# Kernel optimization log

Measured on AMD Instinct MI355X. Metric: run time of the kernel, lower is better.

The kernel has to match this reference:

```python
import jax, jax.numpy as jnp
import numpy as np

T = 2048      # number of utterances in the dialogue (sequential loop dim)
L = 50        # tokens per utterance
V = 30000     # vocab size
D = 300       # word embedding dim
NF = 64       # CNN filters per width
H = 100       # hidden size (hard-coded in CMN)
NC = 7        # emotion classes
WIND = 40     # args.wind1 sliding memory window
HOPS = 3      # args.hops
NEG = -1e10   # masked_fill value in dotprod_attention


def setup_inputs() -> dict:
    key = jax.random.key(0)
    ks = jax.random.split(key, 24)
    s = 0.05

    def n(k, shape):
        return jax.random.normal(k, shape, jnp.float32) * s

    return {
        "sents": jax.random.randint(ks[0], (T, L), 0, V, dtype=jnp.int32),
        "lengths": jax.random.randint(ks[1], (T,), 1, L, dtype=jnp.int32),
        "emb": n(ks[2], (V, D)),
        "Wc3": n(ks[3], (NF, 1, 3, D)), "bc3": n(ks[4], (NF,)),
        "Wc4": n(ks[5], (NF, 1, 4, D)), "bc4": n(ks[6], (NF,)),
        "Wc5": n(ks[7], (NF, 1, 5, D)), "bc5": n(ks[8], (NF,)),
        "Wt": n(ks[9], (3 * NF, H)), "bt": n(ks[10], (H,)),
        "Wih_c": n(ks[11], (3 * H, H)), "Whh_c": n(ks[12], (3 * H, H)),
        "bih_c": n(ks[13], (3 * H,)), "bhh_c": n(ks[14], (3 * H,)),
        "Wih_m": n(ks[15], (3 * H, H)), "Whh_m": n(ks[16], (3 * H, H)),
        "bih_m": n(ks[17], (3 * H,)), "bhh_m": n(ks[18], (3 * H,)),
        "Wcls": n(ks[19], (H, NC)), "bcls": n(ks[20], (NC,)),
    }


def _gru_cell(x, h, Wih, Whh, bih, bhh):
    # torch GRU cell, gate order (r, z, n)
    gi = x @ Wih.T + bih
    gh = h @ Whh.T + bhh
    ir, iz, inn = jnp.split(gi, 3, axis=-1)
    hr, hz, hn = jnp.split(gh, 3, axis=-1)
    r = jax.nn.sigmoid(ir + hr)
    z = jax.nn.sigmoid(iz + hz)
    nw = jnp.tanh(inn + r * hn)
    return (1.0 - z) * nw + z * h


def reference(sents, lengths, emb, Wc3, bc3, Wc4, bc4, Wc5, bc5, Wt, bt,
              Wih_c, Whh_c, bih_c, bhh_c, Wih_m, Whh_m, bih_m, bhh_m,
              Wcls, bcls):
    # ---- CNN utterance encoder (dropout layers are identity in eval) ----
    w = emb[sents]                       # (T, L, D)
    x = w[:, None]                       # (T, 1, L, D)  NCHW
    feats = []
    for Wc, bc in ((Wc3, bc3), (Wc4, bc4), (Wc5, bc5)):
        y = jax.lax.conv_general_dilated(
            x, Wc, window_strides=(1, 1), padding='VALID',
            dimension_numbers=('NCHW', 'OIHW', 'NCHW'))  # (T, NF, L-fs+1, 1)
        feats.append(jnp.max(jax.nn.relu(y + bc[None, :, None, None]), axis=(2, 3)))
    s_utt = jnp.tanh(jnp.concatenate(feats, axis=1) @ Wt + bt)  # (T, H)

    # ---- context GRU over utterances 0..T-2 (hidden after torch step i is hiddens[i-1]) ----
    def cont_step(h, u):
        h2 = _gru_cell(u, h, Wih_c, Whh_c, bih_c, bhh_c)
        return h2, h2
    _, hiddens = jax.lax.scan(cont_step, jnp.zeros((H,), jnp.float32), s_utt[:-1])  # (T-1, H)

    # ---- sliding memory windows: step i (1..T-1) sees hiddens[i-WIND .. i-1], newest last ----
    idx = jnp.arange(1, T)[:, None] - WIND + jnp.arange(WIND)[None, :]  # (T-1, WIND)
    valid = idx >= 0
    mem_all = jnp.where(valid[..., None], hiddens[jnp.clip(idx, 0)], 0.0)  # (T-1, WIND, H)

    def attend(query, mem, v):
        # query: (H,), mem: (WIND, H), v: (WIND,) bool
        for _ in range(HOPS):
            scores = jnp.where(v, mem @ query, NEG)
            a = jax.nn.softmax(scores)
            query = jnp.tanh(query + a @ mem)
            if HOPS > 1:
                # mem_gru over the valid suffix of the window (zero init hidden,
                # padded slots skipped so recurrence starts at first valid slot)
                def mstep(hm, xv):
                    xx, vv = xv
                    hn = _gru_cell(xx, hm, Wih_m, Whh_m, bih_m, bhh_m)
                    hm = jnp.where(vv, hn, hm)
                    return hm, hm
                _, mem = jax.lax.scan(mstep, jnp.zeros((H,), jnp.float32), (mem, v))
        return query

    queries = jax.vmap(attend)(s_utt[1:], mem_all, valid)       # (T-1, H)
    s_cont = jnp.concatenate([s_utt[:1], queries], axis=0)      # (T, H)
    logits = s_cont @ Wcls + bcls                                # (T, NC)
    return jax.nn.log_softmax(logits, axis=1)
```

## Files before the change

kernel.cpp:

```cpp
#include <hip/hip_runtime.h>

#define TT 2048
#define LL 50
#define DD 300
#define HH 100
#define NCC 7

typedef unsigned short u16;
typedef unsigned int u32;
typedef _Float16 f16x2 __attribute__((ext_vector_type(2)));
typedef _Float16 f16x8 __attribute__((ext_vector_type(8)));
typedef float f32x4 __attribute__((ext_vector_type(4)));

__device__ __forceinline__ float frcp(float x){ return __builtin_amdgcn_rcpf(x); }
__device__ __forceinline__ float sigm(float x){ return frcp(1.f + __expf(-x)); }
__device__ __forceinline__ float ftanh(float x){ return 1.f - 2.f * frcp(1.f + __expf(2.f * x)); }

#if defined(__has_builtin)
#if __has_builtin(__builtin_amdgcn_fdot2)
#define HAS_FDOT2 1
#endif
#endif
__device__ __forceinline__ float fdot2(f16x2 a, f16x2 b, float c){
#ifdef HAS_FDOT2
  return __builtin_amdgcn_fdot2(a, b, c, false);
#else
  return c + (float)a.x * (float)b.x + (float)a.y * (float)b.y;
#endif
}
__device__ __forceinline__ f16x2 pk(float x, float y){ f16x2 r; r.x = (_Float16)x; r.y = (_Float16)y; return r; }

__global__ __launch_bounds__(256) void k_prep(const float* __restrict__ Wc3,
    const float* __restrict__ Wc4, const float* __restrict__ Wc5, _Float16* __restrict__ wtp)
{
  const int t = blockIdx.x;
  int kki, ntile, kt;
  if (t < 120){ kki = 0; ntile = t / 30;        kt = t % 30; }
  else if (t < 280){ kki = 1; int r = t - 120; ntile = r / 40; kt = r % 40; }
  else { kki = 2; int r = t - 280;             ntile = r / 50; kt = r % 50; }
  const float* W = (kki == 0) ? Wc3 : ((kki == 1) ? Wc4 : Wc5);
  const int kk = 3 + kki;
  #pragma unroll
  for (int u = 0; u < 2; ++u){
    int e = threadIdx.x * 2 + u;
    int lane = e >> 3, i = e & 7;
    int k = kt * 32 + (lane >> 4) * 8 + i;
    int f = ntile * 16 + (lane & 15);
    int j = k / 320, d = k - j * 320;
    float v = (d < DD) ? W[((size_t)f * kk + j) * DD + d] : 0.f;
    wtp[(size_t)t * 512 + e] = (_Float16)v;
  }
}

#define WST 328
__global__ __launch_bounds__(256) void k_cnn(const int* __restrict__ sents,
    const float* __restrict__ emb, const _Float16* __restrict__ wtp,
    const float* __restrict__ bc3, const float* __restrict__ bc4, const float* __restrict__ bc5,
    const float* __restrict__ Wt,  const float* __restrict__ bt,
    float* __restrict__ su)
{
  __shared__ __attribute__((aligned(16))) _Float16 w16[52 * WST];
  __shared__ float feats[192];
  __shared__ int ids[LL];
  const int tid = threadIdx.x;
  const int s = blockIdx.x;

  if (tid < LL) ids[tid] = sents[s * LL + tid];
  for (int e = tid; e < 52 * WST / 2; e += 256) ((u32*)w16)[e] = 0u;
  __syncthreads();
  for (int e = tid; e < LL * 75; e += 256){
    int l = e / 75, d4 = (e - l * 75) * 4;
    float4 v = *(const float4*)&emb[(size_t)ids[l] * DD + d4];
    _Float16* p = &w16[l * WST + d4];
    p[0] = (_Float16)v.x; p[1] = (_Float16)v.y; p[2] = (_Float16)v.z; p[3] = (_Float16)v.w;
  }
  __syncthreads();

  const int lane = tid & 63, wid = tid >> 6;
  const int rl = lane & 15, gp = lane >> 4;
  const int kkstart[3] = {0, 120, 280};
  float fmaxv[3];
  #pragma unroll
  for (int kki = 0; kki < 3; ++kki){
    const int kk = 3 + kki, nkt = kk * 10, Pk = LL - kk + 1;
    f32x4 acc0 = {0.f,0.f,0.f,0.f}, acc1 = acc0, acc2 = acc0;
    const f16x8* bp = (const f16x8*)(wtp + (size_t)(kkstart[kki] + wid * nkt) * 512) + lane;
    int j = 0, d = gp * 8;
    for (int kt = 0; kt < nkt; ++kt){
      f16x8 b  = bp[(size_t)kt * 64];
      f16x8 a0 = *(const f16x8*)&w16[(rl      + j) * WST + d];
      f16x8 a1 = *(const f16x8*)&w16[(16 + rl + j) * WST + d];
      f16x8 a2 = *(const f16x8*)&w16[(32 + rl + j) * WST + d];
      acc0 = __builtin_amdgcn_mfma_f32_16x16x32_f16(a0, b, acc0, 0, 0, 0);
      acc1 = __builtin_amdgcn_mfma_f32_16x16x32_f16(a1, b, acc1, 0, 0, 0);
      acc2 = __builtin_amdgcn_mfma_f32_16x16x32_f16(a2, b, acc2, 0, 0, 0);
      d += 32; if (d >= 320){ d -= 320; ++j; }
    }
    float m = -1e30f;
    #pragma unroll
    for (int r = 0; r < 4; ++r){
      int p0 = gp * 4 + r;
      if (p0 < Pk)      m = fmaxf(m, acc0[r]);
      if (16 + p0 < Pk) m = fmaxf(m, acc1[r]);
      if (32 + p0 < Pk) m = fmaxf(m, acc2[r]);
    }
    m = fmaxf(m, __shfl_xor(m, 16));
    m = fmaxf(m, __shfl_xor(m, 32));
    fmaxv[kki] = m;
  }
  if (lane < 16){
    feats[  0 + wid * 16 + lane] = fmaxv[0];
    feats[ 64 + wid * 16 + lane] = fmaxv[1];
    feats[128 + wid * 16 + lane] = fmaxv[2];
  }
  __syncthreads();
  if (tid < 192){
    float bias = (tid < 64) ? bc3[tid] : ((tid < 128) ? bc4[tid - 64] : bc5[tid - 128]);
    feats[tid] = fmaxf(0.f, feats[tid] + bias);
  }
  __syncthreads();
  if (tid < HH){
    float acc = bt[tid];
    for (int c = 0; c < 192; ++c)
      acc += feats[c] * Wt[c * HH + tid];
    su[(size_t)s * HH + tid] = ftanh(acc);
  }
}

__global__ __launch_bounds__(320) void k_gi(const float* __restrict__ src,
    const float* __restrict__ W, const float* __restrict__ b, float* __restrict__ dst)
{
  __shared__ float x[HH];
  const int t = blockIdx.x, tid = threadIdx.x;
  if (tid < HH) x[tid] = src[(size_t)t * HH + tid];
  __syncthreads();
  if (tid < 300){
    float acc = b[tid];
    const float* wr = W + (size_t)tid * HH;
    #pragma unroll
    for (int i = 0; i < 25; ++i){
      float4 wv = *(const float4*)(wr + 4 * i);
      float4 xv = *(const float4*)&x[4 * i];
      acc += xv.x * wv.x + xv.y * wv.y + xv.z * wv.z + xv.w * wv.w;
    }
    dst[(size_t)t * 300 + tid] = acc;
  }
}

#define CH 32
__global__ __launch_bounds__(320, 1) void k_scan(const float* __restrict__ gi,
    const float* __restrict__ Whh, const float* __restrict__ bhh,
    float* __restrict__ hid, int steps)
{
  __shared__ __attribute__((aligned(16))) _Float16 h16[128];
  __shared__ __attribute__((aligned(16))) float gh_l[304];
  __shared__ float gi_buf[CH * 300];
  __shared__ float hid_buf[CH * HH];
  const int tid = threadIdx.x;
  const int lane = tid & 63, wvid = tid >> 6;
  const int rl = lane & 15, gp = lane >> 4;

  f16x8 afrag[4][4];
  #pragma unroll
  for (int m = 0; m < 4; ++m){
    int mt = wvid + 5 * m;
    int row = mt * 16 + rl;
    #pragma unroll
    for (int kt = 0; kt < 4; ++kt){
      f16x8 f;
      #pragma unroll
      for (int i = 0; i < 8; ++i){
        int k = kt * 32 + gp * 8 + i;
        float v = (row < 300 && k < 100) ? Whh[(size_t)row * 100 + k] : 0.f;
        f[i] = (_Float16)v;
      }
      afrag[m][kt] = f;
    }
  }
  float bhr = 0.f, bhz = 0.f, bhn = 0.f, hreg = 0.f;
  if (tid < HH){ bhr = bhh[tid]; bhz = bhh[tid + 100]; bhn = bhh[tid + 200]; }
  if (tid < 128) h16[tid] = (_Float16)0.f;
  {
    int c0 = (steps < CH ? steps : CH) * 75;
    for (int e = tid; e < c0; e += 320)
      ((float4*)gi_buf)[e] = ((const float4*)gi)[e];
  }
  __syncthreads();

  int t0 = 0;
  while (t0 < steps){
    int cnt = steps - t0; if (cnt > CH) cnt = CH;
    for (int s = 0; s < cnt; ++s){
      {
        const f16x8* hp = (const f16x8*)h16;
        f16x8 bf0 = hp[ 0 + gp], bf1 = hp[ 4 + gp], bf2 = hp[ 8 + gp], bf3 = hp[12 + gp];
        #pragma unroll
        for (int m = 0; m < 4; ++m){
          f32x4 acc = {0.f, 0.f, 0.f, 0.f};
          acc = __builtin_amdgcn_mfma_f32_16x16x32_f16(afrag[m][0], bf0, acc, 0, 0, 0);
          acc = __builtin_amdgcn_mfma_f32_16x16x32_f16(afrag[m][1], bf1, acc, 0, 0, 0);
          acc = __builtin_amdgcn_mfma_f32_16x16x32_f16(afrag[m][2], bf2, acc, 0, 0, 0);
          acc = __builtin_amdgcn_mfma_f32_16x16x32_f16(afrag[m][3], bf3, acc, 0, 0, 0);
          int mt = wvid + 5 * m;
          if (rl == 0 && mt < 19)
            *(float4*)&gh_l[mt * 16 + gp * 4] = *(float4*)&acc;
        }
      }
      __syncthreads();
      if (tid < HH){
        const float* gpp = gi_buf + s * 300;
        float r = sigm(gpp[tid]       + gh_l[tid]       + bhr);
        float z = sigm(gpp[tid + 100] + gh_l[tid + 100] + bhz);
        float n = ftanh(gpp[tid + 200] + r * (gh_l[tid + 200] + bhn));
        float o = (1.f - z) * n + z * hreg;
        hreg = o;
        h16[tid] = (_Float16)o;
        hid_buf[s * HH + tid] = o;
      }
      __syncthreads();
    }
    for (int e = tid; e < cnt * 25; e += 320)
      ((float4*)(hid + (size_t)t0 * HH))[e] = ((const float4*)hid_buf)[e];
    int nt0 = t0 + cnt;
    int ncnt = steps - nt0; if (ncnt > CH) ncnt = CH; if (ncnt < 0) ncnt = 0;
    for (int e = tid; e < ncnt * 75; e += 320)
      ((float4*)gi_buf)[e] = ((const float4*)(gi + (size_t)nt0 * 300))[e];
    __syncthreads();
    t0 = nt0;
  }
}

__global__ __launch_bounds__(320) void k_att(
    const float* __restrict__ su, const float* __restrict__ hid, const float* __restrict__ gm,
    const float* __restrict__ Wih, const float* __restrict__ Whh,
    const float* __restrict__ bih, const float* __restrict__ bhh,
    float* __restrict__ scont)
{
  __shared__ float mem_l[40 * 104];
  __shared__ __attribute__((aligned(16))) _Float16 mem16[40 * 104];
  __shared__ float hbuf[HH];
  __shared__ __attribute__((aligned(16))) _Float16 hb16[104];
  __shared__ float gh_l[300];
  __shared__ float q_l[104];
  __shared__ float sc_l[40];
  __shared__ float bi_l[300];
  __shared__ _Float16 g_l[40 * 300];
  const int tid = threadIdx.x;
  const int q = blockIdx.x;
  int wmin = 39 - q; if (wmin < 0) wmin = 0;
  f16x2 wreg[52];
  float bh = 0.f;

  if (tid < 300){ bi_l[tid] = bih[tid]; bh = bhh[tid]; }
  if (tid < 104) q_l[tid] = (tid < 100) ? su[(size_t)(q + 1) * HH + tid] : 0.f;
  for (int e = tid; e < 40 * 104; e += 320){
    int w = e / 104, i = e - w * 104;
    float v = 0.f;
    if (i < 100 && w >= wmin) v = hid[(size_t)(q - 39 + w) * HH + i];
    mem_l[e] = v;
    mem16[e] = (_Float16)v;
  }
  for (int e = tid; e < 40 * 300; e += 320){
    int w = e / 300, j = e - w * 300;
    float v = (w >= wmin) ? gm[(size_t)(q - 39 + w) * 300 + j] : 0.f;
    g_l[e] = (_Float16)v;
  }
  if (tid < 300){
    const float* r0 = Whh + (size_t)tid * 100;
    #pragma unroll
    for (int i = 0; i < 25; ++i){
      float4 a = *(const float4*)(r0 + 4 * i);
      wreg[2*i] = pk(a.x, a.y); wreg[2*i+1] = pk(a.z, a.w);
    }
  }
  wreg[50] = pk(0,0); wreg[51] = pk(0,0);
  __syncthreads();

  for (int hop = 0; hop < 3; ++hop){
    if (tid < 40){
      float a0 = 0, a1 = 0, a2 = 0, a3 = 0;
      const float* mr = &mem_l[tid * 104];
      #pragma unroll
      for (int i = 0; i < 25; ++i){
        float4 m4 = *(const float4*)&mr[4 * i];
        float4 q4 = *(const float4*)&q_l[4 * i];
        a0 += m4.x * q4.x; a1 += m4.y * q4.y; a2 += m4.z * q4.z; a3 += m4.w * q4.w;
      }
      sc_l[tid] = (tid >= wmin) ? ((a0 + a1) + (a2 + a3)) : -1e10f;
    }
    __syncthreads();
    if (tid < 64){
      float v = (tid < 40) ? sc_l[tid] : -3e38f;
      float m = v;
      #pragma unroll
      for (int off = 32; off; off >>= 1) m = fmaxf(m, __shfl_xor(m, off));
      float e = (tid < 40) ? __expf(v - m) : 0.f;
      float ssum = e;
      #pragma unroll
      for (int off = 32; off; off >>= 1) ssum += __shfl_xor(ssum, off);
      if (tid < 40) sc_l[tid] = e * frcp(ssum);
    }
    __syncthreads();
    if (tid < 50){
      float c0 = 0.f, c1 = 0.f;
      for (int w = wmin; w < 40; ++w){
        float a = sc_l[w];
        float2 mv = *(const float2*)&mem_l[w * 104 + 2 * tid];
        c0 += a * mv.x; c1 += a * mv.y;
      }
      float q0 = ftanh(q_l[2 * tid]     + c0);
      float q1 = ftanh(q_l[2 * tid + 1] + c1);
      *(float2*)&q_l[2 * tid] = make_float2(q0, q1);
      if (hop == 2)
        *(float2*)&scont[(size_t)(q + 1) * HH + 2 * tid] = make_float2(q0, q1);
    }
    if (hop == 2) break;

    if (hop == 1){
      if (tid < 300){
        const float* r0 = Wih + (size_t)tid * 100;
        #pragma unroll
        for (int i = 0; i < 25; ++i){
          float4 a = *(const float4*)(r0 + 4 * i);
          wreg[2*i] = pk(a.x, a.y); wreg[2*i+1] = pk(a.z, a.w);
        }
        for (int w = 0; w < 40; ++w){
          float a0 = 0, a1 = 0;
          const float4* mq = (const float4*)&mem16[w * 104];
          #pragma unroll
          for (int g = 0; g < 13; ++g){
            float4 hv = mq[g];
            a0 = fdot2(wreg[4*g  ], __builtin_bit_cast(f16x2, hv.x), a0);
            a1 = fdot2(wreg[4*g+1], __builtin_bit_cast(f16x2, hv.y), a1);
            a0 = fdot2(wreg[4*g+2], __builtin_bit_cast(f16x2, hv.z), a0);
            a1 = fdot2(wreg[4*g+3], __builtin_bit_cast(f16x2, hv.w), a1);
          }
          g_l[w * 300 + tid] = (_Float16)(a0 + a1 + bi_l[tid]);
        }
        const float* rh = Whh + (size_t)tid * 100;
        #pragma unroll
        for (int i = 0; i < 25; ++i){
          float4 a = *(const float4*)(rh + 4 * i);
          wreg[2*i] = pk(a.x, a.y); wreg[2*i+1] = pk(a.z, a.w);
        }
      }
    }

    if (tid < HH) hbuf[tid] = 0.f;
    if (tid < 104) hb16[tid] = (_Float16)0.f;
    __syncthreads();
    for (int w = 0; w < 40; ++w){
      if (tid < 300){
        float a0 = 0, a1 = 0;
        const float4* hq = (const float4*)hb16;
        #pragma unroll
        for (int g = 0; g < 13; ++g){
          float4 hv = hq[g];
          a0 = fdot2(wreg[4*g  ], __builtin_bit_cast(f16x2, hv.x), a0);
          a1 = fdot2(wreg[4*g+1], __builtin_bit_cast(f16x2, hv.y), a1);
          a0 = fdot2(wreg[4*g+2], __builtin_bit_cast(f16x2, hv.z), a0);
          a1 = fdot2(wreg[4*g+3], __builtin_bit_cast(f16x2, hv.w), a1);
        }
        gh_l[tid] = a0 + a1 + bh;
      }
      __syncthreads();
      if (tid < HH){
        float o = hbuf[tid];
        if (w >= wmin){
          const _Float16* gp = &g_l[w * 300];
          float gir = (float)gp[tid], giz = (float)gp[tid + 100], gin = (float)gp[tid + 200];
          float r = sigm(gir + gh_l[tid]);
          float z = sigm(giz + gh_l[tid + 100]);
          float n = ftanh(gin + r * gh_l[tid + 200]);
          o = (1.f - z) * n + z * o;
        }
        hbuf[tid] = o;
        hb16[tid] = (_Float16)o;
        mem_l[w * 104 + tid] = o;
        mem16[w * 104 + tid] = (_Float16)o;
      }
      __syncthreads();
    }
  }
}

__global__ __launch_bounds__(256) void k_cls(const float* __restrict__ su, const float* __restrict__ scont,
    const float* __restrict__ Wcls, const float* __restrict__ bcls, float* __restrict__ out)
{
  __shared__ float wl[HH * NCC];
  __shared__ float bl[NCC];
  const int tid = threadIdx.x;
  for (int e = tid; e < HH * NCC; e += 256) wl[e] = Wcls[e];
  if (tid < NCC) bl[tid] = bcls[tid];
  __syncthreads();
  int r = blockIdx.x * 256 + tid;
  if (r < TT){
    const float* v = (r == 0) ? su : (scont + (size_t)r * HH);
    float l[NCC];
    #pragma unroll
    for (int c = 0; c < NCC; ++c) l[c] = bl[c];
    for (int h = 0; h < HH; ++h){
      float x = v[h];
      #pragma unroll
      for (int c = 0; c < NCC; ++c) l[c] += x * wl[h * NCC + c];
    }
    float m = l[0];
    #pragma unroll
    for (int c = 1; c < NCC; ++c) m = fmaxf(m, l[c]);
    float ssum = 0.f;
    #pragma unroll
    for (int c = 0; c < NCC; ++c) ssum += __expf(l[c] - m);
    float lse = m + __logf(ssum);
    #pragma unroll
    for (int c = 0; c < NCC; ++c) out[(size_t)r * NCC + c] = l[c] - lse;
  }
}

extern "C" void kernel_launch(void* const* d_in, const int* in_sizes, int n_in,
                              void* d_out, int out_size, void* d_ws, size_t ws_size,
                              hipStream_t stream)
{
  const int* sents  = (const int*)d_in[0];
  const float* emb    = (const float*)d_in[2];
  const float* Wc3    = (const float*)d_in[3];  const float* bc3 = (const float*)d_in[4];
  const float* Wc4    = (const float*)d_in[5];  const float* bc4 = (const float*)d_in[6];
  const float* Wc5    = (const float*)d_in[7];  const float* bc5 = (const float*)d_in[8];
  const float* Wt     = (const float*)d_in[9];  const float* bt  = (const float*)d_in[10];
  const float* Wih_c  = (const float*)d_in[11]; const float* Whh_c = (const float*)d_in[12];
  const float* bih_c  = (const float*)d_in[13]; const float* bhh_c = (const float*)d_in[14];
  const float* Wih_m  = (const float*)d_in[15]; const float* Whh_m = (const float*)d_in[16];
  const float* bih_m  = (const float*)d_in[17]; const float* bhh_m = (const float*)d_in[18];
  const float* Wcls   = (const float*)d_in[19]; const float* bcls  = (const float*)d_in[20];

  float* ws    = (float*)d_ws;
  float* su    = ws;
  float* gic   = su  + 204800;
  float* hid   = gic + 614100;
  float* gm    = gic;
  float* scont = hid + 204700;
  _Float16* wtp = (_Float16*)(scont + 204800);

  k_prep<<<480,     256, 0, stream>>>(Wc3, Wc4, Wc5, wtp);
  k_cnn <<<TT,      256, 0, stream>>>(sents, emb, wtp, bc3, bc4, bc5, Wt, bt, su);
  k_gi  <<<TT - 1,  320, 0, stream>>>(su, Wih_c, bih_c, gic);
  k_scan<<<1,       320, 0, stream>>>(gic, Whh_c, bhh_c, hid, TT - 1);
  k_gi  <<<TT - 1,  320, 0, stream>>>(hid, Wih_m, bih_m, gm);
  k_att <<<TT - 1,  320, 0, stream>>>(su, hid, gm, Wih_m, Whh_m, bih_m, bhh_m, scont);
  k_cls <<<(TT + 255) / 256, 256, 0, stream>>>(su, scont, Wcls, bcls, (float*)d_out);
}
```

Before: 2.011 ms.

## Interleave GRU gate rows so each lane computes its hidden unit from MFMA output

Reorders the Whh rows loaded into MFMA A-fragments so each 4-row group holds the r, z and n rows of one hidden unit. Each lane can then finish the GRU gate math straight from its accumulator registers instead of staging gh through shared memory. The hidden state is double-buffered, which drops one __syncthreads per recurrent step. In exchange every wave issues 20 MFMAs per step instead of 16, and the gate math is computed redundantly across lanes.

Result: slower. 2.435 ms (+21.1%).

```diff
diff --git a/kernel.cpp b/kernel.cpp
--- a/kernel.cpp
+++ b/kernel.cpp
@@ -152,34 +152,36 @@
     const float* __restrict__ Whh, const float* __restrict__ bhh,
     float* __restrict__ hid, int steps)
 {
-  __shared__ __attribute__((aligned(16))) _Float16 h16[128];
-  __shared__ __attribute__((aligned(16))) float gh_l[304];
+  __shared__ __attribute__((aligned(16))) _Float16 hA[128];
+  __shared__ __attribute__((aligned(16))) _Float16 hB[128];
   __shared__ float gi_buf[CH * 300];
   __shared__ float hid_buf[CH * HH];
   const int tid = threadIdx.x;
   const int lane = tid & 63, wvid = tid >> 6;
   const int rl = lane & 15, gp = lane >> 4;
 
-  f16x8 afrag[4][4];
+  f16x8 afrag[5][4];
   #pragma unroll
-  for (int m = 0; m < 4; ++m){
-    int mt = wvid + 5 * m;
-    int row = mt * 16 + rl;
+  for (int m = 0; m < 5; ++m){
+    const int mt = wvid * 5 + m;
+    const int uu = mt * 4 + (rl >> 2), g = rl & 3;
     #pragma unroll
     for (int kt = 0; kt < 4; ++kt){
       f16x8 f;
       #pragma unroll
       for (int i = 0; i < 8; ++i){
         int k = kt * 32 + gp * 8 + i;
-        float v = (row < 300 && k < 100) ? Whh[(size_t)row * 100 + k] : 0.f;
+        float v = (g < 3 && k < 100) ? Whh[(size_t)(uu + 100 * g) * 100 + k] : 0.f;
         f[i] = (_Float16)v;
       }
       afrag[m][kt] = f;
     }
   }
-  float bhr = 0.f, bhz = 0.f, bhn = 0.f, hreg = 0.f;
-  if (tid < HH){ bhr = bhh[tid]; bhz = bhh[tid + 100]; bhn = bhh[tid + 200]; }
-  if (tid < 128) h16[tid] = (_Float16)0.f;
+  const int msel = rl % 5;
+  const int u = wvid * 20 + msel * 4 + gp;
+  const float bhr = bhh[u], bhz = bhh[u + 100], bhn = bhh[u + 200];
+  float hreg = 0.f;
+  if (tid < 128){ hA[tid] = (_Float16)0.f; hB[tid] = (_Float16)0.f; }
   {
     int c0 = (steps < CH ? steps : CH) * 75;
     for (int e = tid; e < c0; e += 320)
@@ -191,31 +193,46 @@
   while (t0 < steps){
     int cnt = steps - t0; if (cnt > CH) cnt = CH;
     for (int s = 0; s < cnt; ++s){
-      {
-        const f16x8* hp = (const f16x8*)h16;
-        f16x8 bf0 = hp[ 0 + gp], bf1 = hp[ 4 + gp], bf2 = hp[ 8 + gp], bf3 = hp[12 + gp];
-        #pragma unroll
-        for (int m = 0; m < 4; ++m){
-          f32x4 acc = {0.f, 0.f, 0.f, 0.f};
-          acc = __builtin_amdgcn_mfma_f32_16x16x32_f16(afrag[m][0], bf0, acc, 0, 0, 0);
-          acc = __builtin_amdgcn_mfma_f32_16x16x32_f16(afrag[m][1], bf1, acc, 0, 0, 0);
-          acc = __builtin_amdgcn_mfma_f32_16x16x32_f16(afrag[m][2], bf2, acc, 0, 0, 0);
-          acc = __builtin_amdgcn_mfma_f32_16x16x32_f16(afrag[m][3], bf3, acc, 0, 0, 0);
-          int mt = wvid + 5 * m;
-          if (rl == 0 && mt < 19)
-            *(float4*)&gh_l[mt * 16 + gp * 4] = *(float4*)&acc;
-        }
-      }
-      __syncthreads();
-      if (tid < HH){
-        const float* gpp = gi_buf + s * 300;
-        float r = sigm(gpp[tid]       + gh_l[tid]       + bhr);
-        float z = sigm(gpp[tid + 100] + gh_l[tid + 100] + bhz);
-        float n = ftanh(gpp[tid + 200] + r * (gh_l[tid + 200] + bhn));
-        float o = (1.f - z) * n + z * hreg;
-        hreg = o;
-        h16[tid] = (_Float16)o;
-        hid_buf[s * HH + tid] = o;
+      const int st = t0 + s;
+      const _Float16* hs = (st & 1) ? hB : hA;
+      _Float16*       hd = (st & 1) ? hA : hB;
+      float gir = gi_buf[s * 300 + u];
+      float giz = gi_buf[s * 300 + 100 + u];
+      float gin = gi_buf[s * 300 + 200 + u];
+      const f16x8* hp = (const f16x8*)hs;
+      f16x8 bf0 = hp[0 + gp], bf1 = hp[4 + gp], bf2 = hp[8 + gp], bf3 = hp[12 + gp];
+      f32x4 a0 = {0.f,0.f,0.f,0.f}, a1 = a0, a2 = a0, a3 = a0, a4 = a0;
+      a0 = __builtin_amdgcn_mfma_f32_16x16x32_f16(afrag[0][0], bf0, a0, 0, 0, 0);
+      a1 = __builtin_amdgcn_mfma_f32_16x16x32_f16(afrag[1][0], bf0, a1, 0, 0, 0);
+      a2 = __builtin_amdgcn_mfma_f32_16x16x32_f16(afrag[2][0], bf0, a2, 0, 0, 0);
+      a3 = __builtin_amdgcn_mfma_f32_16x16x32_f16(afrag[3][0], bf0, a3, 0, 0, 0);
+      a4 = __builtin_amdgcn_mfma_f32_16x16x32_f16(afrag[4][0], bf0, a4, 0, 0, 0);
+      a0 = __builtin_amdgcn_mfma_f32_16x16x32_f16(afrag[0][1], bf1, a0, 0, 0, 0);
+      a1 = __builtin_amdgcn_mfma_f32_16x16x32_f16(afrag[1][1], bf1, a1, 0, 0, 0);
+      a2 = __builtin_amdgcn_mfma_f32_16x16x32_f16(afrag[2][1], bf1, a2, 0, 0, 0);
+      a3 = __builtin_amdgcn_mfma_f32_16x16x32_f16(afrag[3][1], bf1, a3, 0, 0, 0);
+      a4 = __builtin_amdgcn_mfma_f32_16x16x32_f16(afrag[4][1], bf1, a4, 0, 0, 0);
+      a0 = __builtin_amdgcn_mfma_f32_16x16x32_f16(afrag[0][2], bf2, a0, 0, 0, 0);
+      a1 = __builtin_amdgcn_mfma_f32_16x16x32_f16(afrag[1][2], bf2, a1, 0, 0, 0);
+      a2 = __builtin_amdgcn_mfma_f32_16x16x32_f16(afrag[2][2], bf2, a2, 0, 0, 0);
+      a3 = __builtin_amdgcn_mfma_f32_16x16x32_f16(afrag[3][2], bf2, a3, 0, 0, 0);
+      a4 = __builtin_amdgcn_mfma_f32_16x16x32_f16(afrag[4][2], bf2, a4, 0, 0, 0);
+      a0 = __builtin_amdgcn_mfma_f32_16x16x32_f16(afrag[0][3], bf3, a0, 0, 0, 0);
+      a1 = __builtin_amdgcn_mfma_f32_16x16x32_f16(afrag[1][3], bf3, a1, 0, 0, 0);
+      a2 = __builtin_amdgcn_mfma_f32_16x16x32_f16(afrag[2][3], bf3, a2, 0, 0, 0);
+      a3 = __builtin_amdgcn_mfma_f32_16x16x32_f16(afrag[3][3], bf3, a3, 0, 0, 0);
+      a4 = __builtin_amdgcn_mfma_f32_16x16x32_f16(afrag[4][3], bf3, a4, 0, 0, 0);
+      float ghr = msel==0 ? a0[0] : msel==1 ? a1[0] : msel==2 ? a2[0] : msel==3 ? a3[0] : a4[0];
+      float ghz = msel==0 ? a0[1] : msel==1 ? a1[1] : msel==2 ? a2[1] : msel==3 ? a3[1] : a4[1];
+      float ghn = msel==0 ? a0[2] : msel==1 ? a1[2] : msel==2 ? a2[2] : msel==3 ? a3[2] : a4[2];
+      float r = sigm(gir + ghr + bhr);
+      float z = sigm(giz + ghz + bhz);
+      float n = ftanh(gin + r * (ghn + bhn));
+      float o = (1.f - z) * n + z * hreg;
+      hreg = o;
+      if (rl < 5){
+        hd[u] = (_Float16)o;
+        hid_buf[s * HH + u] = o;
       }
       __syncthreads();
     }
```

## Batch eight queries per block in attention kernel and run memory GRU on MFMA

Applied to the files above, without the earlier changes.

The per-query attention kernel is replaced by one that handles eight queries per block. Their memory-GRU recurrences are batched into 16x16x32 f16 MFMA matmuls, with Whh held in registers in a pre-packed MFMA layout produced by a new prep kernel. The hop-1 input projection also moves to MFMA, using chunked staging of gate inputs and a double-buffered hidden state in shared memory. This is meant to replace the many tiny per-block fdot2 matvecs and their 40 sequential syncs per hop with fewer, denser matrix ops. In exchange, memory is now stored in f16, which loosens precision, and launching 256 blocks at one block per CU limits parallelism.

After: 1.744 ms. 13.3% less time.

```diff
diff --git a/kernel.cpp b/kernel.cpp
--- a/kernel.cpp
+++ b/kernel.cpp
@@ -9,6 +9,7 @@
 typedef unsigned short u16;
 typedef unsigned int u32;
 typedef _Float16 f16x2 __attribute__((ext_vector_type(2)));
+typedef _Float16 f16x4 __attribute__((ext_vector_type(4)));
 typedef _Float16 f16x8 __attribute__((ext_vector_type(8)));
 typedef float f32x4 __attribute__((ext_vector_type(4)));
 
@@ -49,6 +50,22 @@
     int j = k / 320, d = k - j * 320;
     float v = (d < DD) ? W[((size_t)f * kk + j) * DD + d] : 0.f;
     wtp[(size_t)t * 512 + e] = (_Float16)v;
+  }
+}
+
+__global__ __launch_bounds__(256) void k_prep2(const float* __restrict__ Whh,
+    const float* __restrict__ Wih, _Float16* __restrict__ wpkW, _Float16* __restrict__ wpkI)
+{
+  const float* W = (blockIdx.x == 0) ? Whh : Wih;
+  _Float16* dst  = (blockIdx.x == 0) ? wpkW : wpkI;
+  for (int idx = threadIdx.x; idx < 28 * 4 * 64 * 8; idx += 256){
+    int i = idx & 7, lane = (idx >> 3) & 63, kt = (idx >> 9) & 3, mt = idx >> 11;
+    int rl = lane & 15, gp = lane >> 4;
+    int p = mt * 16 + rl;
+    int k = kt * 32 + gp * 8 + i;
+    int uu = p >> 2, g = p & 3;
+    float v = (mt < 25 && g < 3 && k < 100) ? W[(size_t)(uu + 100 * g) * 100 + k] : 0.f;
+    dst[idx] = (_Float16)v;
   }
 }
 
@@ -230,156 +247,209 @@
   }
 }
 
-__global__ __launch_bounds__(320) void k_att(
+__global__ __launch_bounds__(256, 1) void k_att2(
     const float* __restrict__ su, const float* __restrict__ hid, const float* __restrict__ gm,
-    const float* __restrict__ Wih, const float* __restrict__ Whh,
+    const _Float16* __restrict__ wpkW, const _Float16* __restrict__ wpkI,
     const float* __restrict__ bih, const float* __restrict__ bhh,
     float* __restrict__ scont)
 {
-  __shared__ float mem_l[40 * 104];
-  __shared__ __attribute__((aligned(16))) _Float16 mem16[40 * 104];
-  __shared__ float hbuf[HH];
-  __shared__ __attribute__((aligned(16))) _Float16 hb16[104];
-  __shared__ float gh_l[300];
-  __shared__ float q_l[104];
-  __shared__ float sc_l[40];
-  __shared__ float bi_l[300];
-  __shared__ _Float16 g_l[40 * 300];
+  __shared__ __attribute__((aligned(16))) _Float16 MEM[40][8][136];
+  __shared__ __attribute__((aligned(16))) _Float16 H16[2][8][136];
+  __shared__ __attribute__((aligned(16))) _Float16 GI2[8][8][100][4];
+  __shared__ float QL[8][104];
+  __shared__ float SC[8][40];
+
   const int tid = threadIdx.x;
-  const int q = blockIdx.x;
-  int wmin = 39 - q; if (wmin < 0) wmin = 0;
-  f16x2 wreg[52];
-  float bh = 0.f;
-
-  if (tid < 300){ bi_l[tid] = bih[tid]; bh = bhh[tid]; }
-  if (tid < 104) q_l[tid] = (tid < 100) ? su[(size_t)(q + 1) * HH + tid] : 0.f;
-  for (int e = tid; e < 40 * 104; e += 320){
-    int w = e / 104, i = e - w * 104;
-    float v = 0.f;
-    if (i < 100 && w >= wmin) v = hid[(size_t)(q - 39 + w) * HH + i];
-    mem_l[e] = v;
-    mem16[e] = (_Float16)v;
-  }
-  for (int e = tid; e < 40 * 300; e += 320){
-    int w = e / 300, j = e - w * 300;
-    float v = (w >= wmin) ? gm[(size_t)(q - 39 + w) * 300 + j] : 0.f;
-    g_l[e] = (_Float16)v;
-  }
-  if (tid < 300){
-    const float* r0 = Whh + (size_t)tid * 100;
-    #pragma unroll
-    for (int i = 0; i < 25; ++i){
-      float4 a = *(const float4*)(r0 + 4 * i);
-      wreg[2*i] = pk(a.x, a.y); wreg[2*i+1] = pk(a.z, a.w);
-    }
-  }
-  wreg[50] = pk(0,0); wreg[51] = pk(0,0);
+  const int lane = tid & 63, wvid = tid >> 6;
+  const int rl = lane & 15, gp = lane >> 4;
+  const int qbase = blockIdx.x * 8;
+  const int j = rl & 7;
+  const int qi = qbase + j;
+  int wminj = 39 - qi; if (wminj < 0) wminj = 0;
+  if (qi >= TT - 1) wminj = 40;
+
+  f16x8 aW[7][4];
+  #pragma unroll
+  for (int t = 0; t < 7; ++t){
+    int mt = wvid + 4 * t;
+    #pragma unroll
+    for (int kt = 0; kt < 4; ++kt)
+      aW[t][kt] = *(const f16x8*)(wpkW + (size_t)((mt * 4 + kt) * 64 + lane) * 8);
+  }
+  float bi_[7][3];
+  #pragma unroll
+  for (int t = 0; t < 7; ++t){
+    int mt = wvid + 4 * t;
+    bool v = (mt < 25);
+    int uu = v ? (mt * 4 + gp) : 0;
+    bi_[t][0] = v ? bih[uu]       : 0.f;
+    bi_[t][1] = v ? bih[uu + 100] : 0.f;
+    bi_[t][2] = v ? bih[uu + 200] : 0.f;
+  }
+  const int cbase = (rl < 8) ? 0 : 4;
+  float bh_[4][3]; int cu[4]; bool cv[4];
+  #pragma unroll
+  for (int tt = 0; tt < 4; ++tt){
+    int t = cbase + tt;
+    int mt = wvid + 4 * t;
+    bool v = (t < 7) && (mt < 25);
+    cv[tt] = v;
+    int uu = v ? (mt * 4 + gp) : 0;
+    cu[tt] = uu;
+    bh_[tt][0] = v ? bhh[uu]       : 0.f;
+    bh_[tt][1] = v ? bhh[uu + 100] : 0.f;
+    bh_[tt][2] = v ? bhh[uu + 200] : 0.f;
+  }
+
+  for (int e = tid; e < 40 * 8 * 34; e += 256){
+    int i4 = e % 34, wj = e / 34, w = wj >> 3, jj = wj & 7;
+    int qq = qbase + jj;
+    int row = qq - 39 + w;
+    f16x4 v4 = {0, 0, 0, 0};
+    if (i4 < 25 && qq < TT - 1 && row >= 0){
+      float4 f = *(const float4*)&hid[(size_t)row * HH + i4 * 4];
+      v4[0] = (_Float16)f.x; v4[1] = (_Float16)f.y; v4[2] = (_Float16)f.z; v4[3] = (_Float16)f.w;
+    }
+    *(f16x4*)&MEM[w][jj][i4 * 4] = v4;
+  }
+  for (int e = tid; e < 8 * 104; e += 256){
+    int jj = e / 104, ii = e % 104;
+    int qq = qbase + jj;
+    QL[jj][ii] = (ii < 100 && qq < TT - 1) ? su[(size_t)(qq + 1) * HH + ii] : 0.f;
+  }
+  for (int e = tid; e < 2 * 8 * 136; e += 256) ((_Float16*)H16)[e] = (_Float16)0;
   __syncthreads();
 
   for (int hop = 0; hop < 3; ++hop){
-    if (tid < 40){
-      float a0 = 0, a1 = 0, a2 = 0, a3 = 0;
-      const float* mr = &mem_l[tid * 104];
-      #pragma unroll
-      for (int i = 0; i < 25; ++i){
-        float4 m4 = *(const float4*)&mr[4 * i];
-        float4 q4 = *(const float4*)&q_l[4 * i];
-        a0 += m4.x * q4.x; a1 += m4.y * q4.y; a2 += m4.z * q4.z; a3 += m4.w * q4.w;
-      }
-      sc_l[tid] = (tid >= wmin) ? ((a0 + a1) + (a2 + a3)) : -1e10f;
-    }
-    __syncthreads();
-    if (tid < 64){
-      float v = (tid < 40) ? sc_l[tid] : -3e38f;
-      float m = v;
-      #pragma unroll
-      for (int off = 32; off; off >>= 1) m = fmaxf(m, __shfl_xor(m, off));
-      float e = (tid < 40) ? __expf(v - m) : 0.f;
-      float ssum = e;
-      #pragma unroll
-      for (int off = 32; off; off >>= 1) ssum += __shfl_xor(ssum, off);
-      if (tid < 40) sc_l[tid] = e * frcp(ssum);
-    }
-    __syncthreads();
-    if (tid < 50){
-      float c0 = 0.f, c1 = 0.f;
-      for (int w = wmin; w < 40; ++w){
-        float a = sc_l[w];
-        float2 mv = *(const float2*)&mem_l[w * 104 + 2 * tid];
-        c0 += a * mv.x; c1 += a * mv.y;
-      }
-      float q0 = ftanh(q_l[2 * tid]     + c0);
-      float q1 = ftanh(q_l[2 * tid + 1] + c1);
-      *(float2*)&q_l[2 * tid] = make_float2(q0, q1);
-      if (hop == 2)
-        *(float2*)&scont[(size_t)(q + 1) * HH + 2 * tid] = make_float2(q0, q1);
-    }
-    if (hop == 2) break;
-
-    if (hop == 1){
-      if (tid < 300){
-        const float* r0 = Wih + (size_t)tid * 100;
-        #pragma unroll
-        for (int i = 0; i < 25; ++i){
-          float4 a = *(const float4*)(r0 + 4 * i);
-          wreg[2*i] = pk(a.x, a.y); wreg[2*i+1] = pk(a.z, a.w);
-        }
-        for (int w = 0; w < 40; ++w){
-          float a0 = 0, a1 = 0;
-          const float4* mq = (const float4*)&mem16[w * 104];
-          #pragma unroll
-          for (int g = 0; g < 13; ++g){
-            float4 hv = mq[g];
-            a0 = fdot2(wreg[4*g  ], __builtin_bit_cast(f16x2, hv.x), a0);
-            a1 = fdot2(wreg[4*g+1], __builtin_bit_cast(f16x2, hv.y), a1);
-            a0 = fdot2(wreg[4*g+2], __builtin_bit_cast(f16x2, hv.z), a0);
-            a1 = fdot2(wreg[4*g+3], __builtin_bit_cast(f16x2, hv.w), a1);
-          }
-          g_l[w * 300 + tid] = (_Float16)(a0 + a1 + bi_l[tid]);
-        }
-        const float* rh = Whh + (size_t)tid * 100;
-        #pragma unroll
-        for (int i = 0; i < 25; ++i){
-          float4 a = *(const float4*)(rh + 4 * i);
-          wreg[2*i] = pk(a.x, a.y); wreg[2*i+1] = pk(a.z, a.w);
-        }
-      }
-    }
-
-    if (tid < HH) hbuf[tid] = 0.f;
-    if (tid < 104) hb16[tid] = (_Float16)0.f;
-    __syncthreads();
-    for (int w = 0; w < 40; ++w){
-      if (tid < 300){
-        float a0 = 0, a1 = 0;
-        const float4* hq = (const float4*)hb16;
+    for (int e = tid; e < 320; e += 256){
+      int jj = e / 40, w = e % 40;
+      int qq = qbase + jj;
+      int wm = 39 - qq; if (wm < 0) wm = 0; if (qq >= TT - 1) wm = 40;
+      float acc = 0.f;
+      if (w >= wm){
         #pragma unroll
         for (int g = 0; g < 13; ++g){
-          float4 hv = hq[g];
-          a0 = fdot2(wreg[4*g  ], __builtin_bit_cast(f16x2, hv.x), a0);
-          a1 = fdot2(wreg[4*g+1], __builtin_bit_cast(f16x2, hv.y), a1);
-          a0 = fdot2(wreg[4*g+2], __builtin_bit_cast(f16x2, hv.z), a0);
-          a1 = fdot2(wreg[4*g+3], __builtin_bit_cast(f16x2, hv.w), a1);
+          f16x8 m8 = *(const f16x8*)&MEM[w][jj][g * 8];
+          const float* qp = &QL[jj][g * 8];
+          #pragma unroll
+          for (int i = 0; i < 8; ++i) acc += (float)m8[i] * qp[i];
         }
-        gh_l[tid] = a0 + a1 + bh;
+        SC[jj][w] = acc;
+      } else SC[jj][w] = -1e10f;
+    }
+    __syncthreads();
+    if (tid < 8){
+      float m = -3e38f;
+      for (int w = 0; w < 40; ++w) m = fmaxf(m, SC[tid][w]);
+      float s = 0.f;
+      for (int w = 0; w < 40; ++w){ float e = __expf(SC[tid][w] - m); SC[tid][w] = e; s += e; }
+      float inv = frcp(s);
+      for (int w = 0; w < 40; ++w) SC[tid][w] *= inv;
+    }
+    __syncthreads();
+    for (int e = tid; e < 400; e += 256){
+      int jj = e / 50, i2 = e % 50;
+      float c0 = 0.f, c1 = 0.f;
+      for (int w = 0; w < 40; ++w){
+        float a = SC[jj][w];
+        f16x2 m2 = *(const f16x2*)&MEM[w][jj][i2 * 2];
+        c0 += a * (float)m2.x; c1 += a * (float)m2.y;
+      }
+      float q0 = ftanh(QL[jj][i2 * 2]     + c0);
+      float q1 = ftanh(QL[jj][i2 * 2 + 1] + c1);
+      QL[jj][i2 * 2] = q0; QL[jj][i2 * 2 + 1] = q1;
+      if (hop == 2){
+        int qq = qbase + jj;
+        if (qq < TT - 1)
+          *(float2*)&scont[(size_t)(qq + 1) * HH + i2 * 2] = make_float2(q0, q1);
+      }
+    }
+    if (hop == 2) break;
+    for (int e = tid; e < 800; e += 256) H16[0][e / 100][e % 100] = (_Float16)0;
+    float hrg[4] = {0.f, 0.f, 0.f, 0.f};
+    __syncthreads();
+
+    for (int c = 0; c < 5; ++c){
+      if (hop == 0){
+        for (int e = tid; e < 6400; e += 256){
+          int s8 = e / 800, jj = (e / 100) & 7, uu = e % 100;
+          int qq = qbase + jj;
+          int row = qq - 39 + c * 8 + s8;
+          f16x4 g4 = {0, 0, 0, 0};
+          if (qq < TT - 1 && row >= 0){
+            const float* gr = &gm[(size_t)row * 300];
+            g4[0] = (_Float16)gr[uu]; g4[1] = (_Float16)gr[uu + 100]; g4[2] = (_Float16)gr[uu + 200];
+          }
+          *(f16x4*)&GI2[s8][jj][uu][0] = g4;
+        }
+      } else {
+        #pragma unroll
+        for (int nt = 0; nt < 4; ++nt){
+          f16x8 bf[4];
+          #pragma unroll
+          for (int kt = 0; kt < 4; ++kt)
+            bf[kt] = *(const f16x8*)&MEM[c * 8 + nt * 2 + (rl >> 3)][rl & 7][kt * 32 + gp * 8];
+          #pragma unroll
+          for (int t = 0; t < 7; ++t){
+            int mt = wvid + 4 * t;
+            if (mt < 25){
+              f32x4 ac = {0.f, 0.f, 0.f, 0.f};
+              #pragma unroll
+              for (int kt = 0; kt < 4; ++kt){
+                f16x8 ai = *(const f16x8*)(wpkI + (size_t)((mt * 4 + kt) * 64 + lane) * 8);
+                ac = __builtin_amdgcn_mfma_f32_16x16x32_f16(ai, bf[kt], ac, 0, 0, 0);
+              }
+              int uu = mt * 4 + gp;
+              int s8 = nt * 2 + (rl >> 3), jj = rl & 7;
+              f16x4 g4;
+              g4[0] = (_Float16)(ac[0] + bi_[t][0]);
+              g4[1] = (_Float16)(ac[1] + bi_[t][1]);
+              g4[2] = (_Float16)(ac[2] + bi_[t][2]);
+              g4[3] = (_Float16)0.f;
+              *(f16x4*)&GI2[s8][jj][uu][0] = g4;
+            }
+          }
+        }
       }
       __syncthreads();
-      if (tid < HH){
-        float o = hbuf[tid];
-        if (w >= wmin){
-          const _Float16* gp = &g_l[w * 300];
-          float gir = (float)gp[tid], giz = (float)gp[tid + 100], gin = (float)gp[tid + 200];
-          float r = sigm(gir + gh_l[tid]);
-          float z = sigm(giz + gh_l[tid + 100]);
-          float n = ftanh(gin + r * gh_l[tid + 200]);
-          o = (1.f - z) * n + z * o;
+      for (int s = 0; s < 8; ++s){
+        int w = c * 8 + s;
+        const _Float16 (*hs)[136] = H16[w & 1];
+        _Float16 (*hd)[136] = H16[(w + 1) & 1];
+        f16x8 b0 = *(const f16x8*)&hs[j][      gp * 8];
+        f16x8 b1 = *(const f16x8*)&hs[j][32  + gp * 8];
+        f16x8 b2 = *(const f16x8*)&hs[j][64  + gp * 8];
+        f16x8 b3 = *(const f16x8*)&hs[j][96  + gp * 8];
+        f32x4 acc[7];
+        #pragma unroll
+        for (int t = 0; t < 7; ++t){
+          int mt = wvid + 4 * t;
+          f32x4 a = {0.f, 0.f, 0.f, 0.f};
+          if (mt < 25){
+            a = __builtin_amdgcn_mfma_f32_16x16x32_f16(aW[t][0], b0, a, 0, 0, 0);
+            a = __builtin_amdgcn_mfma_f32_16x16x32_f16(aW[t][1], b1, a, 0, 0, 0);
+            a = __builtin_amdgcn_mfma_f32_16x16x32_f16(aW[t][2], b2, a, 0, 0, 0);
+            a = __builtin_amdgcn_mfma_f32_16x16x32_f16(aW[t][3], b3, a, 0, 0, 0);
+          }
+          acc[t] = a;
         }
-        hbuf[tid] = o;
-        hb16[tid] = (_Float16)o;
-        mem_l[w * 104 + tid] = o;
-        mem16[w * 104 + tid] = (_Float16)o;
-      }
-      __syncthreads();
+        const bool vw = (w >= wminj);
+        #pragma unroll
+        for (int tt = 0; tt < 4; ++tt){
+          if (cv[tt]){
+            f32x4 ac = (rl < 8) ? acc[tt] : acc[(tt + 4 < 7) ? (tt + 4) : 6];
+            f16x4 g4 = *(const f16x4*)&GI2[s][j][cu[tt]][0];
+            float r = sigm((float)g4[0] + ac[0] + bh_[tt][0]);
+            float z = sigm((float)g4[1] + ac[1] + bh_[tt][1]);
+            float n = ftanh((float)g4[2] + r * (ac[2] + bh_[tt][2]));
+            float o = vw ? ((1.f - z) * n + z * hrg[tt]) : hrg[tt];
+            hrg[tt] = o;
+            hd[j][cu[tt]]     = (_Float16)o;
+            MEM[w][j][cu[tt]] = (_Float16)o;
+          }
+        }
+        __syncthreads();
+      }
     }
   }
 }
@@ -438,13 +508,16 @@
   float* hid   = gic + 614100;
   float* gm    = gic;
   float* scont = hid + 204700;
-  _Float16* wtp = (_Float16*)(scont + 204800);
-
-  k_prep<<<480,     256, 0, stream>>>(Wc3, Wc4, Wc5, wtp);
-  k_cnn <<<TT,      256, 0, stream>>>(sents, emb, wtp, bc3, bc4, bc5, Wt, bt, su);
-  k_gi  <<<TT - 1,  320, 0, stream>>>(su, Wih_c, bih_c, gic);
-  k_scan<<<1,       320, 0, stream>>>(gic, Whh_c, bhh_c, hid, TT - 1);
-  k_gi  <<<TT - 1,  320, 0, stream>>>(hid, Wih_m, bih_m, gm);
-  k_att <<<TT - 1,  320, 0, stream>>>(su, hid, gm, Wih_m, Whh_m, bih_m, bhh_m, scont);
-  k_cls <<<(TT + 255) / 256, 256, 0, stream>>>(su, scont, Wcls, bcls, (float*)d_out);
-}
+  _Float16* wtp  = (_Float16*)(scont + 204800);
+  _Float16* wpkW = wtp + 245760;
+  _Float16* wpkI = wpkW + 57344;
+
+  k_prep <<<480,    256, 0, stream>>>(Wc3, Wc4, Wc5, wtp);
+  k_prep2<<<2,      256, 0, stream>>>(Whh_m, Wih_m, wpkW, wpkI);
+  k_cnn  <<<TT,     256, 0, stream>>>(sents, emb, wtp, bc3, bc4, bc5, Wt, bt, su);
+  k_gi   <<<TT - 1, 320, 0, stream>>>(su, Wih_c, bih_c, gic);
+  k_scan <<<1,      320, 0, stream>>>(gic, Whh_c, bhh_c, hid, TT - 1);
+  k_gi   <<<TT - 1, 320, 0, stream>>>(hid, Wih_m, bih_m, gm);
+  k_att2 <<<256,    256, 0, stream>>>(su, hid, gm, wpkW, wpkI, bih_m, bhh_m, scont);
+  k_cls  <<<(TT + 255) / 256, 256, 0, stream>>>(su, scont, Wcls, bcls, (float*)d_out);
+}
```
